# Kernel optimization log

Measured on AMD Instinct MI355X. Metric: run time of the kernel, lower is better.

The kernel has to match this reference:

```python
import jax, jax.numpy as jnp
import numpy as np

N_NODES = 100000


def _gcn_conv(x, src, dst, norm, W, b, n):
    # x: [N, F_in]; linear transform then degree-normalized scatter-add aggregation
    h = x @ W                                  # [N, F_out]
    msgs = h[src] * norm[:, None]              # gather + scale, [E', F_out]
    out = jax.ops.segment_sum(msgs, dst, num_segments=n)  # scatter-add
    return out + b


def _norm_and_loops(edge_index, n):
    # add self-loops and compute symmetric normalization deg^-1/2 * deg^-1/2
    loops = jnp.arange(n, dtype=edge_index.dtype)
    src = jnp.concatenate([edge_index[0], loops])
    dst = jnp.concatenate([edge_index[1], loops])
    deg = jax.ops.segment_sum(jnp.ones_like(dst, dtype=jnp.float32), dst, num_segments=n)
    dinv = jnp.where(deg > 0, jax.lax.rsqrt(jnp.maximum(deg, 1.0)), 0.0)
    norm = dinv[src] * dinv[dst]
    return src, dst, norm


def setup_inputs() -> dict:
    key = jax.random.key(0)
    k1, k2, k3, k4, k5 = jax.random.split(key, 5)
    x = jax.random.normal(k1, (N_NODES, 500), dtype=jnp.float32)
    edge_index = jax.random.randint(k2, (2, 3200000), 0, N_NODES, dtype=jnp.int64)
    # Glorot-style init for GCNConv weights
    W1 = jax.random.normal(k3, (500, 16), dtype=jnp.float32) * (1.0 / np.sqrt(500))
    b1 = jnp.zeros((16,), dtype=jnp.float32)
    W2 = jax.random.normal(k4, (16, 3), dtype=jnp.float32) * (1.0 / np.sqrt(16))
    b2 = jnp.zeros((3,), dtype=jnp.float32)
    return {"x": x, "edge_index": edge_index, "W1": W1, "b1": b1, "W2": W2, "b2": b2}


def reference(x, edge_index, W1, b1, W2, b2):
    n = x.shape[0]
    src, dst, norm = _norm_and_loops(edge_index, n)
    h = _gcn_conv(x, src, dst, norm, W1, b1, n)
    h = jax.nn.relu(h)
    # dropout is identity in eval mode (training=False)
    h = _gcn_conv(h, src, dst, norm, W2, b2, n)
    return jax.nn.log_softmax(h, axis=1)
```

## Files before the change

### kernel.cpp

```cpp
#include <hip/hip_runtime.h>
#include <hip/hip_bf16.h>

#define F_IN 500
#define F_HID 16
#define F_OUT 3
#define BN 64
#define CBN 256
#define CE 8192
#define TILE 2048
#define MAXB 512
#define KCH 32
#define GROWS 128

__device__ __forceinline__ int clampi(int v, int lo, int hi) {
    return min(max(v, lo), hi);
}

__device__ __forceinline__ float bf2f(unsigned short u) {
    return __uint_as_float((unsigned)u << 16);
}

__device__ __forceinline__ unsigned short f2bf(float v) {
    __hip_bfloat16 h = __float2bfloat16(v);
    return *reinterpret_cast<unsigned short*>(&h);
}

__global__ __launch_bounds__(1024) void k_passA(const int* __restrict__ ei, int E, int N,
                                                int NCB, int* __restrict__ hist) {
    __shared__ int lh[MAXB];
    int c = blockIdx.x;
    for (int i = threadIdx.x; i < NCB; i += 1024) lh[i] = 0;
    __syncthreads();
    int base = c * CE, lim = min(base + CE, E);
    for (int e = base + (int)threadIdx.x; e < lim; e += 1024) {
        int d = clampi(ei[(size_t)E + e], 0, N - 1);
        atomicAdd(&lh[d >> 8], 1);
    }
    __syncthreads();
    for (int i = threadIdx.x; i < NCB; i += 1024) hist[(size_t)c * NCB + i] = lh[i];
}

__global__ __launch_bounds__(512) void k_scanchunks(int* __restrict__ hist, int NCH,
                                                    int NCB, int* __restrict__ tot) {
    __shared__ int s[512];
    int b = blockIdx.x, t = threadIdx.x;
    int v = (t < NCH) ? hist[(size_t)t * NCB + b] : 0;
    s[t] = v;
    __syncthreads();
    for (int off = 1; off < 512; off <<= 1) {
        int add = (t >= off) ? s[t - off] : 0;
        __syncthreads();
        s[t] += add;
        __syncthreads();
    }
    if (t < NCH) hist[(size_t)t * NCB + b] = s[t] - v;
    if (t == 511) tot[b] = s[511];
}

__global__ __launch_bounds__(512) void k_scanbuckets(const int* __restrict__ tot, int NCB,
                                                     int E, int* __restrict__ cbstart) {
    __shared__ int s[512];
    int t = threadIdx.x;
    int v = (t < NCB) ? tot[t] : 0;
    s[t] = v;
    __syncthreads();
    for (int off = 1; off < 512; off <<= 1) {
        int add = (t >= off) ? s[t - off] : 0;
        __syncthreads();
        s[t] += add;
        __syncthreads();
    }
    if (t < NCB) cbstart[t] = s[t] - v;
    if (t == 0) cbstart[NCB] = E;
}

__global__ __launch_bounds__(1024) void k_passB(const int* __restrict__ ei, int E, int N,
                                                int NCB, const int* __restrict__ hist,
                                                const int* __restrict__ cbstart,
                                                unsigned* __restrict__ ebufC) {
    __shared__ int loff[MAXB];
    __shared__ int lcnt[MAXB];
    int c = blockIdx.x;
    for (int i = threadIdx.x; i < NCB; i += 1024) {
        loff[i] = cbstart[i] + hist[(size_t)c * NCB + i];
        lcnt[i] = 0;
    }
    __syncthreads();
    int base = c * CE, lim = min(base + CE, E);
    for (int e = base + (int)threadIdx.x; e < lim; e += 1024) {
        int s = clampi(ei[e], 0, N - 1);
        int d = clampi(ei[(size_t)E + e], 0, N - 1);
        int b = d >> 8;
        int pos = loff[b] + atomicAdd(&lcnt[b], 1);
        ebufC[pos] = ((unsigned)s << 8) | (unsigned)(d & 255);
    }
}

__global__ __launch_bounds__(1024) void k_passC(const unsigned* __restrict__ ebufC,
                                                const int* __restrict__ cbstart,
                                                unsigned* __restrict__ ebuf2,
                                                int* __restrict__ fbstart,
                                                int* __restrict__ degi, int N) {
    __shared__ int pcnt[CBN];
    __shared__ int soff[4], scur[4];
    int b = blockIdx.x, t = threadIdx.x;
    int cs = cbstart[b], ce = cbstart[b + 1];
    if (t < CBN) pcnt[t] = 0;
    __syncthreads();
    for (int i = cs + t; i < ce; i += 1024) atomicAdd(&pcnt[ebufC[i] & 255], 1);
    __syncthreads();
    if (t == 0) {
        int r = 0;
#pragma unroll
        for (int s = 0; s < 4; ++s) {
            int c = 0;
            for (int j = s * 64; j < s * 64 + 64; ++j) c += pcnt[j];
            soff[s] = r;
            scur[s] = r;
            r += c;
        }
    }
    __syncthreads();
    if (t < 4) fbstart[b * 4 + t] = cs + soff[t];
    int node = b * CBN + t;
    if (t < CBN && node < N) degi[node] = pcnt[t];
    __syncthreads();
    int lane = t & 63;
    unsigned long long ltm = (1ull << lane) - 1ull;
    for (int base = cs; base < ce; base += 1024) {
        int i = base + t;
        bool valid = i < ce;
        unsigned rec = valid ? ebufC[i] : 0u;
        int sub = (rec >> 6) & 3;
        unsigned frec = ((rec >> 8) << 6) | (rec & 63);
        int pos = 0;
        bool have = false;
#pragma unroll
        for (int s = 0; s < 4; ++s) {
            bool mine = valid && (sub == s);
            unsigned long long m = __ballot(mine);
            if (m) {
                int leader = __ffsll((unsigned long long)m) - 1;
                int cnt = __popcll(m);
                int bp = 0;
                if (lane == leader) bp = atomicAdd(&scur[s], cnt);
                bp = __shfl(bp, leader);
                if (mine) {
                    pos = bp + __popcll(m & ltm);
                    have = true;
                }
            }
        }
        if (have) ebuf2[cs + pos] = frec;
    }
}

__global__ void k_dinv(const int* __restrict__ degi, float* __restrict__ dinv, int N) {
    int i = blockIdx.x * blockDim.x + threadIdx.x;
    if (i >= N) return;
    dinv[i] = rsqrtf((float)degi[i] + 1.0f);
}

__global__ __launch_bounds__(GROWS) void k_gemm1(const float* __restrict__ x,
                                                 const float* __restrict__ W1,
                                                 const float* __restrict__ dinv,
                                                 __hip_bfloat16* __restrict__ hs1b, int N) {
    __shared__ float xt[GROWS * KCH];
    const int t = threadIdx.x;
    const int row0 = blockIdx.x * GROWS;
    const int sw = t & 7;

    float acc[F_HID];
#pragma unroll
    for (int j = 0; j < F_HID; ++j) acc[j] = 0.f;

    float4 pf[8];

#define LOADC(c)                                                          \
    {                                                                     \
        _Pragma("unroll")                                                 \
        for (int i = 0; i < 8; ++i) {                                     \
            int f = i * GROWS + t;                                        \
            int r = f >> 3, c4 = f & 7;                                   \
            int gr = row0 + r, gk = (c) * KCH + c4 * 4;                   \
            float4 v = make_float4(0.f, 0.f, 0.f, 0.f);                   \
            if (gr < N && gk < F_IN)                                      \
                v = *(const float4*)(x + (size_t)gr * F_IN + gk);         \
            pf[i] = v;                                                    \
        }                                                                 \
    }

#define STOREC()                                                          \
    {                                                                     \
        _Pragma("unroll")                                                 \
        for (int i = 0; i < 8; ++i) {                                     \
            int f = i * GROWS + t;                                        \
            int r = f >> 3, c4 = f & 7;                                   \
            int slot = c4 ^ (r & 7);                                      \
            *(float4*)(xt + r * KCH + slot * 4) = pf[i];                  \
        }                                                                 \
    }

    LOADC(0);

    for (int c = 0; c < 16; ++c) {
        if (c > 0) __syncthreads();
        STOREC();
        __syncthreads();
        if (c < 15) LOADC(c + 1);

        float4 xld[8];
#pragma unroll
        for (int c4 = 0; c4 < 8; ++c4)
            xld[c4] = *(const float4*)(xt + t * KCH + ((c4 ^ sw) << 2));

        const float* wp = W1 + (size_t)c * KCH * F_HID;
        if (c < 15) {
#pragma unroll
            for (int c4 = 0; c4 < 8; ++c4) {
                float4 xv = xld[c4];
                const float* wr = wp + c4 * 64;
#pragma unroll
                for (int j = 0; j < 16; ++j) acc[j] = fmaf(xv.x, wr[j], acc[j]);
#pragma unroll
                for (int j = 0; j < 16; ++j) acc[j] = fmaf(xv.y, wr[16 + j], acc[j]);
#pragma unroll
                for (int j = 0; j < 16; ++j) acc[j] = fmaf(xv.z, wr[32 + j], acc[j]);
#pragma unroll
                for (int j = 0; j < 16; ++j) acc[j] = fmaf(xv.w, wr[48 + j], acc[j]);
            }
        } else {
#pragma unroll
            for (int c4 = 0; c4 < 5; ++c4) {
                float4 xv = xld[c4];
                const float* wr = wp + c4 * 64;
#pragma unroll
                for (int j = 0; j < 16; ++j) acc[j] = fmaf(xv.x, wr[j], acc[j]);
#pragma unroll
                for (int j = 0; j < 16; ++j) acc[j] = fmaf(xv.y, wr[16 + j], acc[j]);
#pragma unroll
                for (int j = 0; j < 16; ++j) acc[j] = fmaf(xv.z, wr[32 + j], acc[j]);
#pragma unroll
                for (int j = 0; j < 16; ++j) acc[j] = fmaf(xv.w, wr[48 + j], acc[j]);
            }
        }
    }
#undef LOADC
#undef STOREC

    int row = row0 + t;
    if (row < N) {
        float di = dinv[row];
        uint4 u0, u1;
        u0.x = ((unsigned)f2bf(acc[1] * di) << 16) | f2bf(acc[0] * di);
        u0.y = ((unsigned)f2bf(acc[3] * di) << 16) | f2bf(acc[2] * di);
        u0.z = ((unsigned)f2bf(acc[5] * di) << 16) | f2bf(acc[4] * di);
        u0.w = ((unsigned)f2bf(acc[7] * di) << 16) | f2bf(acc[6] * di);
        u1.x = ((unsigned)f2bf(acc[9] * di) << 16) | f2bf(acc[8] * di);
        u1.y = ((unsigned)f2bf(acc[11] * di) << 16) | f2bf(acc[10] * di);
        u1.z = ((unsigned)f2bf(acc[13] * di) << 16) | f2bf(acc[12] * di);
        u1.w = ((unsigned)f2bf(acc[15] * di) << 16) | f2bf(acc[14] * di);
        uint4* dst = (uint4*)((unsigned short*)hs1b + (size_t)row * F_HID);
        dst[0] = u0;
        dst[1] = u1;
    }
}

__global__ __launch_bounds__(256) void k_agg1g2(const unsigned* __restrict__ ebuf2,
                                                const int* __restrict__ bstart,
                                                const __hip_bfloat16* __restrict__ hs1b,
                                                const float* __restrict__ b1,
                                                const float* __restrict__ W2,
                                                const float* __restrict__ dinv,
                                                float* __restrict__ hs2p, int N) {
    __shared__ unsigned rec[TILE];
    __shared__ unsigned srt[TILE];
    __shared__ int cnt[BN], offs[BN], ocur[BN];
    __shared__ float w2s[F_HID * F_OUT];
    __shared__ float b1s[F_HID];
    int b = blockIdx.x, t = threadIdx.x;
    if (t < F_HID * F_OUT) w2s[t] = W2[t];
    if (t < F_HID) b1s[t] = b1[t];
    int s0 = bstart[b], s1 = bstart[b + 1];
    int nl = t >> 2, q = t & 3;
    float ac0 = 0.f, ac1 = 0.f, ac2 = 0.f, ac3 = 0.f;

    for (int tb = s0; tb < s1; tb += TILE) {
        int nv = min(TILE, s1 - tb);
        if (t < BN) cnt[t] = 0;
        for (int i = t; i < nv; i += 256) rec[i] = ebuf2[tb + i];
        __syncthreads();
        for (int i = t; i < nv; i += 256) atomicAdd(&cnt[rec[i] & 63], 1);
        __syncthreads();
        if (t < 64) {
            int v = cnt[t];
            int xp = v;
#pragma unroll
            for (int d = 1; d < 64; d <<= 1) {
                int y = __shfl_up(xp, d);
                if (t >= d) xp += y;
            }
            offs[t] = xp - v;
            ocur[t] = xp - v;
        }
        __syncthreads();
        for (int i = t; i < nv; i += 256) {
            unsigned r = rec[i];
            int pos = atomicAdd(&ocur[r & 63], 1);
            srt[pos] = r >> 6;
        }
        __syncthreads();
        int gs = offs[nl], ge = gs + cnt[nl];
        int i = gs;
        for (; i + 1 < ge; i += 2) {
            unsigned sA = srt[i], sB = srt[i + 1];
            ushort4 uA = *(const ushort4*)(hs1b + (size_t)sA * F_HID + q * 4);
            ushort4 uB = *(const ushort4*)(hs1b + (size_t)sB * F_HID + q * 4);
            ac0 += bf2f(uA.x) + bf2f(uB.x);
            ac1 += bf2f(uA.y) + bf2f(uB.y);
            ac2 += bf2f(uA.z) + bf2f(uB.z);
            ac3 += bf2f(uA.w) + bf2f(uB.w);
        }
        if (i < ge) {
            unsigned sA = srt[i];
            ushort4 uA = *(const ushort4*)(hs1b + (size_t)sA * F_HID + q * 4);
            ac0 += bf2f(uA.x);
            ac1 += bf2f(uA.y);
            ac2 += bf2f(uA.z);
            ac3 += bf2f(uA.w);
        }
        __syncthreads();
    }

    int node = b * BN + nl;
    if (node < N) {
        float di = dinv[node];
        const __hip_bfloat16* hp = hs1b + (size_t)node * F_HID + q * 4;
        ushort4 us = *(const ushort4*)hp;
        float v0 = fmaxf(b1s[q * 4 + 0] + di * (bf2f(us.x) + ac0), 0.f);
        float v1 = fmaxf(b1s[q * 4 + 1] + di * (bf2f(us.y) + ac1), 0.f);
        float v2 = fmaxf(b1s[q * 4 + 2] + di * (bf2f(us.z) + ac2), 0.f);
        float v3 = fmaxf(b1s[q * 4 + 3] + di * (bf2f(us.w) + ac3), 0.f);
        float o0 = v0 * w2s[(q * 4 + 0) * 3 + 0] + v1 * w2s[(q * 4 + 1) * 3 + 0] +
                   v2 * w2s[(q * 4 + 2) * 3 + 0] + v3 * w2s[(q * 4 + 3) * 3 + 0];
        float o1 = v0 * w2s[(q * 4 + 0) * 3 + 1] + v1 * w2s[(q * 4 + 1) * 3 + 1] +
                   v2 * w2s[(q * 4 + 2) * 3 + 1] + v3 * w2s[(q * 4 + 3) * 3 + 1];
        float o2 = v0 * w2s[(q * 4 + 0) * 3 + 2] + v1 * w2s[(q * 4 + 1) * 3 + 2] +
                   v2 * w2s[(q * 4 + 2) * 3 + 2] + v3 * w2s[(q * 4 + 3) * 3 + 2];
        o0 += __shfl_xor(o0, 1); o0 += __shfl_xor(o0, 2);
        o1 += __shfl_xor(o1, 1); o1 += __shfl_xor(o1, 2);
        o2 += __shfl_xor(o2, 1); o2 += __shfl_xor(o2, 2);
        if (q == 0) {
            float4 r = make_float4(o0 * di, o1 * di, o2 * di, 0.f);
            *(float4*)(hs2p + (size_t)node * 4) = r;
        }
    }
}

__global__ __launch_bounds__(256) void k_agg2lsm(const unsigned* __restrict__ ebuf2,
                                                 const int* __restrict__ bstart,
                                                 const float* __restrict__ hs2p,
                                                 const float* __restrict__ b2,
                                                 const float* __restrict__ dinv,
                                                 float* __restrict__ out, int N) {
    __shared__ unsigned rec[TILE];
    __shared__ unsigned srt[TILE];
    __shared__ int cnt[BN], offs[BN], ocur[BN];
    int b = blockIdx.x, t = threadIdx.x;
    int s0 = bstart[b], s1 = bstart[b + 1];
    int nl = t >> 2, c = t & 3;
    float acc = 0.f;

    for (int tb = s0; tb < s1; tb += TILE) {
        int nv = min(TILE, s1 - tb);
        if (t < BN) cnt[t] = 0;
        for (int i = t; i < nv; i += 256) rec[i] = ebuf2[tb + i];
        __syncthreads();
        for (int i = t; i < nv; i += 256) atomicAdd(&cnt[rec[i] & 63], 1);
        __syncthreads();
        if (t < 64) {
            int v = cnt[t];
            int xp = v;
#pragma unroll
            for (int d = 1; d < 64; d <<= 1) {
                int y = __shfl_up(xp, d);
                if (t >= d) xp += y;
            }
            offs[t] = xp - v;
            ocur[t] = xp - v;
        }
        __syncthreads();
        for (int i = t; i < nv; i += 256) {
            unsigned r = rec[i];
            int pos = atomicAdd(&ocur[r & 63], 1);
            srt[pos] = r >> 6;
        }
        __syncthreads();
        int gs = offs[nl], ge = gs + cnt[nl];
        int i = gs;
        for (; i + 1 < ge; i += 2) {
            unsigned sA = srt[i], sB = srt[i + 1];
            acc += hs2p[(size_t)sA * 4 + c] + hs2p[(size_t)sB * 4 + c];
        }
        if (i < ge) acc += hs2p[(size_t)srt[i] * 4 + c];
        __syncthreads();
    }

    int node = b * BN + nl;
    if (node < N) {
        float di = dinv[node];
        float self = hs2p[(size_t)node * 4 + c];
        float bc = (c < 3) ? b2[c] : 0.f;
        float a = bc + di * (self + acc);
        int wbase = (t & 63) & ~3;
        float a0 = __shfl(a, wbase + 0);
        float a1 = __shfl(a, wbase + 1);
        float a2 = __shfl(a, wbase + 2);
        if (c < 3) {
            float m = fmaxf(a0, fmaxf(a1, a2));
            float l = logf(expf(a0 - m) + expf(a1 - m) + expf(a2 - m));
            out[(size_t)node * 3 + c] = a - m - l;
        }
    }
}

extern "C" void kernel_launch(void* const* d_in, const int* in_sizes, int n_in,
                              void* d_out, int out_size, void* d_ws, size_t ws_size,
                              hipStream_t stream) {
    const float* x = (const float*)d_in[0];
    const int* ei = (const int*)d_in[1];
    const float* W1 = (const float*)d_in[2];
    const float* b1 = (const float*)d_in[3];
    const float* W2 = (const float*)d_in[4];
    const float* b2 = (const float*)d_in[5];
    float* out = (float*)d_out;

    const int N = in_sizes[0] / F_IN;
    const int E = in_sizes[1] / 2;
    const int NCB = (N + CBN - 1) / CBN;
    const int NFB = (N + BN - 1) / BN;
    const int NCH = (E + CE - 1) / CE;

    char* p = (char*)d_ws;
    auto alloc = [&](size_t bytes) {
        char* r = p;
        p += (bytes + 255) & ~(size_t)255;
        return r;
    };
    int*            degi    = (int*)alloc((size_t)N * 4);
    float*          dinv    = (float*)alloc((size_t)N * 4);
    int*            hist    = (int*)alloc((size_t)NCH * NCB * 4);
    int*            tot     = (int*)alloc((size_t)NCB * 4);
    int*            cbstart = (int*)alloc(((size_t)NCB + 1) * 4);
    int*            fbstart = (int*)alloc(((size_t)NCB * 4 + 1) * 4);
    unsigned*       ebufC   = (unsigned*)alloc((size_t)E * 4);
    unsigned*       ebuf2   = (unsigned*)alloc((size_t)E * 4);
    __hip_bfloat16* hs1b    = (__hip_bfloat16*)alloc((size_t)N * F_HID * 2);
    float*          hs2p    = (float*)alloc((size_t)N * 4 * 4);

    k_passA<<<NCH, 1024, 0, stream>>>(ei, E, N, NCB, hist);
    k_scanchunks<<<NCB, 512, 0, stream>>>(hist, NCH, NCB, tot);
    k_scanbuckets<<<1, 512, 0, stream>>>(tot, NCB, E, cbstart);
    k_passB<<<NCH, 1024, 0, stream>>>(ei, E, N, NCB, hist, cbstart, ebufC);
    k_passC<<<NCB, 1024, 0, stream>>>(ebufC, cbstart, ebuf2, fbstart, degi, N);
    k_dinv<<<(N + 255) / 256, 256, 0, stream>>>(degi, dinv, N);
    k_gemm1<<<(N + GROWS - 1) / GROWS, GROWS, 0, stream>>>(x, W1, dinv, hs1b, N);
    k_agg1g2<<<NFB, 256, 0, stream>>>(ebuf2, fbstart, hs1b, b1, W2, dinv, hs2p, N);
    k_agg2lsm<<<NFB, 256, 0, stream>>>(ebuf2, fbstart, hs2p, b2, dinv, out, N);
}
```

Measured before the change: 166.6 us.

## Split GEMM1 over K into two halves and fold dinv computation into passC

Computes dinv directly in passC, which drops the separate k_dinv kernel and the degi buffer. GEMM1 now launches twice as many blocks, each covering half of the K dimension, and writes fp32 partial sums. A new combine kernel adds the two halves, scales by dinv and converts to bf16. The aim is more parallelism and occupancy for the 200 MB x read (782 blocks becomes 1564). The cost is an extra 12.8 MB partial-sum round trip and one more kernel launch.

```diff
diff --git a/kernel.cpp b/kernel.cpp
--- a/kernel.cpp
+++ b/kernel.cpp
@@ -100,7 +100,7 @@
                                                 const int* __restrict__ cbstart,
                                                 unsigned* __restrict__ ebuf2,
                                                 int* __restrict__ fbstart,
-                                                int* __restrict__ degi, int N) {
+                                                float* __restrict__ dinv, int N) {
     __shared__ int pcnt[CBN];
     __shared__ int soff[4], scur[4];
     int b = blockIdx.x, t = threadIdx.x;
@@ -123,7 +123,7 @@
     __syncthreads();
     if (t < 4) fbstart[b * 4 + t] = cs + soff[t];
     int node = b * CBN + t;
-    if (t < CBN && node < N) degi[node] = pcnt[t];
+    if (t < CBN && node < N) dinv[node] = rsqrtf((float)pcnt[t] + 1.0f);
     __syncthreads();
     int lane = t & 63;
     unsigned long long ltm = (1ull << lane) - 1ull;
@@ -155,19 +155,15 @@
     }
 }
 
-__global__ void k_dinv(const int* __restrict__ degi, float* __restrict__ dinv, int N) {
-    int i = blockIdx.x * blockDim.x + threadIdx.x;
-    if (i >= N) return;
-    dinv[i] = rsqrtf((float)degi[i] + 1.0f);
-}
-
-__global__ __launch_bounds__(GROWS) void k_gemm1(const float* __restrict__ x,
-                                                 const float* __restrict__ W1,
-                                                 const float* __restrict__ dinv,
-                                                 __hip_bfloat16* __restrict__ hs1b, int N) {
+__global__ __launch_bounds__(GROWS) void k_gemm1s(const float* __restrict__ x,
+                                                  const float* __restrict__ W1,
+                                                  float* __restrict__ hpart, int N) {
     __shared__ float xt[GROWS * KCH];
     const int t = threadIdx.x;
-    const int row0 = blockIdx.x * GROWS;
+    const int nb = blockIdx.x >> 1;
+    const int h = blockIdx.x & 1;
+    const int row0 = nb * GROWS;
+    const int c0 = h * 8;
     const int sw = t & 7;
 
     float acc[F_HID];
@@ -201,13 +197,13 @@
         }                                                                 \
     }
 
-    LOADC(0);
-
-    for (int c = 0; c < 16; ++c) {
-        if (c > 0) __syncthreads();
+    LOADC(c0);
+
+    for (int c = c0; c < c0 + 8; ++c) {
+        if (c > c0) __syncthreads();
         STOREC();
         __syncthreads();
-        if (c < 15) LOADC(c + 1);
+        if (c < c0 + 7) LOADC(c + 1);
 
         float4 xld[8];
 #pragma unroll
@@ -250,20 +246,29 @@
 
     int row = row0 + t;
     if (row < N) {
-        float di = dinv[row];
-        uint4 u0, u1;
-        u0.x = ((unsigned)f2bf(acc[1] * di) << 16) | f2bf(acc[0] * di);
-        u0.y = ((unsigned)f2bf(acc[3] * di) << 16) | f2bf(acc[2] * di);
-        u0.z = ((unsigned)f2bf(acc[5] * di) << 16) | f2bf(acc[4] * di);
-        u0.w = ((unsigned)f2bf(acc[7] * di) << 16) | f2bf(acc[6] * di);
-        u1.x = ((unsigned)f2bf(acc[9] * di) << 16) | f2bf(acc[8] * di);
-        u1.y = ((unsigned)f2bf(acc[11] * di) << 16) | f2bf(acc[10] * di);
-        u1.z = ((unsigned)f2bf(acc[13] * di) << 16) | f2bf(acc[12] * di);
-        u1.w = ((unsigned)f2bf(acc[15] * di) << 16) | f2bf(acc[14] * di);
-        uint4* dst = (uint4*)((unsigned short*)hs1b + (size_t)row * F_HID);
-        dst[0] = u0;
-        dst[1] = u1;
-    }
+        float* dst = hpart + ((size_t)h * N + row) * F_HID;
+        *(float4*)(dst + 0) = make_float4(acc[0], acc[1], acc[2], acc[3]);
+        *(float4*)(dst + 4) = make_float4(acc[4], acc[5], acc[6], acc[7]);
+        *(float4*)(dst + 8) = make_float4(acc[8], acc[9], acc[10], acc[11]);
+        *(float4*)(dst + 12) = make_float4(acc[12], acc[13], acc[14], acc[15]);
+    }
+}
+
+__global__ __launch_bounds__(256) void k_gemm1c(const float* __restrict__ hpart,
+                                                const float* __restrict__ dinv,
+                                                __hip_bfloat16* __restrict__ hs1b, int N) {
+    int g = blockIdx.x * 256 + threadIdx.x;
+    if (g >= N * 4) return;
+    int row = g >> 2;
+    float4 a = ((const float4*)hpart)[g];
+    float4 b = ((const float4*)hpart)[(size_t)N * 4 + g];
+    float di = dinv[row];
+    ushort4 o;
+    o.x = f2bf((a.x + b.x) * di);
+    o.y = f2bf((a.y + b.y) * di);
+    o.z = f2bf((a.z + b.z) * di);
+    o.w = f2bf((a.w + b.w) * di);
+    ((ushort4*)hs1b)[g] = o;
 }
 
 __global__ __launch_bounds__(256) void k_agg1g2(const unsigned* __restrict__ ebuf2,
@@ -447,7 +452,6 @@
         p += (bytes + 255) & ~(size_t)255;
         return r;
     };
-    int*            degi    = (int*)alloc((size_t)N * 4);
     float*          dinv    = (float*)alloc((size_t)N * 4);
     int*            hist    = (int*)alloc((size_t)NCH * NCB * 4);
     int*            tot     = (int*)alloc((size_t)NCB * 4);
@@ -455,6 +459,7 @@
     int*            fbstart = (int*)alloc(((size_t)NCB * 4 + 1) * 4);
     unsigned*       ebufC   = (unsigned*)alloc((size_t)E * 4);
     unsigned*       ebuf2   = (unsigned*)alloc((size_t)E * 4);
+    float*          hpart   = (float*)alloc((size_t)2 * N * F_HID * 4);
     __hip_bfloat16* hs1b    = (__hip_bfloat16*)alloc((size_t)N * F_HID * 2);
     float*          hs2p    = (float*)alloc((size_t)N * 4 * 4);
 
@@ -462,9 +467,9 @@
     k_scanchunks<<<NCB, 512, 0, stream>>>(hist, NCH, NCB, tot);
     k_scanbuckets<<<1, 512, 0, stream>>>(tot, NCB, E, cbstart);
     k_passB<<<NCH, 1024, 0, stream>>>(ei, E, N, NCB, hist, cbstart, ebufC);
-    k_passC<<<NCB, 1024, 0, stream>>>(ebufC, cbstart, ebuf2, fbstart, degi, N);
-    k_dinv<<<(N + 255) / 256, 256, 0, stream>>>(degi, dinv, N);
-    k_gemm1<<<(N + GROWS - 1) / GROWS, GROWS, 0, stream>>>(x, W1, dinv, hs1b, N);
+    k_passC<<<NCB, 1024, 0, stream>>>(ebufC, cbstart, ebuf2, fbstart, dinv, N);
+    k_gemm1s<<<2 * ((N + GROWS - 1) / GROWS), GROWS, 0, stream>>>(x, W1, hpart, N);
+    k_gemm1c<<<(N * 4 + 255) / 256, 256, 0, stream>>>(hpart, dinv, hs1b, N);
     k_agg1g2<<<NFB, 256, 0, stream>>>(ebuf2, fbstart, hs1b, b1, W2, dinv, hs2p, N);
     k_agg2lsm<<<NFB, 256, 0, stream>>>(ebuf2, fbstart, hs2p, b2, dinv, out, N);
 }
```

After: 191.7 us. +15.0%, slower.
